# Kernel optimization log

Hardware: AMD Instinct MI355X
Metric: run time of the kernel (lower is better)

## Reference

```python
import jax, jax.numpy as jnp
import numpy as np

B, S, D, H = 4, 2048, 1024, 16
HD = D // H  # head_dim = 64


def setup_inputs() -> dict:
    key = jax.random.key(0)
    ks = jax.random.split(key, 10)
    scale = 1.0 / np.sqrt(D)
    x = jax.random.normal(ks[0], (B, S, D), dtype=jnp.float32)
    mask = jax.random.randint(ks[1], (B, S, S), 0, 2, dtype=jnp.int32)
    Wq = jax.random.normal(ks[2], (D, D), dtype=jnp.float32) * scale
    Wk = jax.random.normal(ks[3], (D, D), dtype=jnp.float32) * scale
    Wv = jax.random.normal(ks[4], (D, D), dtype=jnp.float32) * scale
    Wo = jax.random.normal(ks[5], (D, D), dtype=jnp.float32) * scale
    bq = jax.random.normal(ks[6], (D,), dtype=jnp.float32) * 0.01
    bk = jax.random.normal(ks[7], (D,), dtype=jnp.float32) * 0.01
    bv = jax.random.normal(ks[8], (D,), dtype=jnp.float32) * 0.01
    bo = jax.random.normal(ks[9], (D,), dtype=jnp.float32) * 0.01
    return {"x": x, "mask": mask, "Wq": Wq, "bq": bq, "Wk": Wk, "bk": bk,
            "Wv": Wv, "bv": bv, "Wo": Wo, "bo": bo}


def reference(x, mask, Wq, bq, Wk, bk, Wv, bv, Wo, bo):
    # QKV projections (nn.Linear: x @ W^T + b; W stored pre-transposed here as [D,D])
    q = x @ Wq + bq  # [B,S,D]
    k = x @ Wk + bk
    v = x @ Wv + bv
    # split heads -> [B,H,S,HD]
    def heads(t):
        return t.reshape(B, S, H, HD).transpose(0, 2, 1, 3)
    q, k, v = heads(q), heads(k), heads(v)
    scores = jnp.einsum('bhqd,bhkd->bhqk', q, k) / jnp.sqrt(jnp.float32(HD))
    # mask: [B,S,S] -> broadcast over heads; positions where mask==0 get -inf
    scores = jnp.where(mask[:, None, :, :] == 0, -jnp.inf, scores)
    attn = jax.nn.softmax(scores, axis=-1)
    attn = jnp.where(jnp.isnan(attn), 0.0, attn)  # nan_to_num(nan=0.0)
    out = jnp.einsum('bhqk,bhkd->bhqd', attn, v)  # [B,H,S,HD]
    out = out.transpose(0, 2, 1, 3).reshape(B, S, D)
    return out @ Wo + bo
```

## Files before the change

### kernel.cpp

```cpp
#include <hip/hip_runtime.h>
#include <hip/hip_bf16.h>
#include <stdint.h>

#define B_  4
#define S_  2048
#define D_  1024
#define H_  16
#define HD_ 64

typedef __attribute__((ext_vector_type(4))) float f32x4;
typedef __attribute__((ext_vector_type(8))) short bf16x8;

typedef const unsigned int __attribute__((address_space(1)))* gas_ptr;
typedef unsigned int __attribute__((address_space(3)))* las_ptr;

__device__ __forceinline__ void async16(const void* g, void* l) {
  __builtin_amdgcn_global_load_lds((gas_ptr)g, (las_ptr)l, 16, 0, 0);
}

__global__ __launch_bounds__(256) void cvt_x(const float* __restrict__ in,
                                             __hip_bfloat16* __restrict__ out,
                                             int n) {
  const int i = (blockIdx.x * blockDim.x + threadIdx.x) * 4;
  if (i >= n) return;
  const float4 v = *(const float4*)(in + i);
  union { ushort4 u; __hip_bfloat16 h[4]; } o;
  o.h[0] = (__hip_bfloat16)v.x;
  o.h[1] = (__hip_bfloat16)v.y;
  o.h[2] = (__hip_bfloat16)v.z;
  o.h[3] = (__hip_bfloat16)v.w;
  *(ushort4*)(out + i) = o.u;
}

__global__ __launch_bounds__(256) void pack_mask(const int* __restrict__ mk,
                                                 unsigned long long* __restrict__ bits) {
  const long long i = (long long)blockIdx.x * 256 + threadIdx.x;
  const unsigned long long b = __ballot(mk[i] != 0);
  if ((threadIdx.x & 63) == 0) bits[i >> 6] = b;
}

__global__ void transpose_w(const float* __restrict__ Wq,
                            const float* __restrict__ Wk,
                            const float* __restrict__ Wv,
                            const float* __restrict__ Wo,
                            __hip_bfloat16* __restrict__ Wt_qkv,
                            __hip_bfloat16* __restrict__ Wt_o) {
  __shared__ float t[32][33];
  const int z = blockIdx.z;
  const float* W = (z == 0) ? Wq : (z == 1) ? Wk : (z == 2) ? Wv : Wo;
  __hip_bfloat16* Wt = (z < 3) ? (Wt_qkv + (size_t)z * D_ * D_) : Wt_o;
  const int x = blockIdx.x * 32 + threadIdx.x;
  const int y = blockIdx.y * 32 + threadIdx.y;
  t[threadIdx.y][threadIdx.x] = W[(size_t)y * D_ + x];
  __syncthreads();
  const int xo = blockIdx.y * 32 + threadIdx.x;
  const int yo = blockIdx.x * 32 + threadIdx.y;
  Wt[(size_t)yo * D_ + xo] = (__hip_bfloat16)t[threadIdx.x][threadIdx.y];
}

__global__ __launch_bounds__(256) void gemm_qkv(
    const __hip_bfloat16* __restrict__ A,
    const __hip_bfloat16* __restrict__ Bt,
    const float* __restrict__ bq,
    const float* __restrict__ bk,
    const float* __restrict__ bv,
    __hip_bfloat16* __restrict__ QKo,
    __hip_bfloat16* __restrict__ Vt) {
  __shared__ __hip_bfloat16 sA[128 * 32];
  __shared__ __hip_bfloat16 sB[128 * 32];
  const int K = 1024;
  const int tid  = threadIdx.x;
  const int wave = tid >> 6;
  const int lane = tid & 63;
  const int quad = lane >> 4;
  const int l16  = lane & 15;
  const int bm = blockIdx.y * 128;
  const int bn = blockIdx.x * 128;
  const int wm = (wave >> 1) * 64;
  const int wn = (wave & 1) * 64;

  const int r0 = wave * 2, r1 = wave * 2 + 1;
  const int lrow = lane >> 2;
  const int lcol = (lane & 3) * 8;

  const __hip_bfloat16* ga0 = A  + (size_t)(bm + r0 * 16 + lrow) * K + lcol;
  const __hip_bfloat16* ga1 = A  + (size_t)(bm + r1 * 16 + lrow) * K + lcol;
  const __hip_bfloat16* gb0 = Bt + (size_t)(bn + r0 * 16 + lrow) * K + lcol;
  const __hip_bfloat16* gb1 = Bt + (size_t)(bn + r1 * 16 + lrow) * K + lcol;
  char* la0 = (char*)sA + r0 * 1024;
  char* la1 = (char*)sA + r1 * 1024;
  char* lb0 = (char*)sB + r0 * 1024;
  char* lb1 = (char*)sB + r1 * 1024;

  const char* pa = (const char*)sA + (wm + l16) * 64 + quad * 16;
  const char* pb = (const char*)sB + (wn + l16) * 64 + quad * 16;

  f32x4 acc[4][4] = {};

  for (int k0 = 0; k0 < K; k0 += 32) {
    async16(ga0 + k0, la0);
    async16(ga1 + k0, la1);
    async16(gb0 + k0, lb0);
    async16(gb1 + k0, lb1);
    __syncthreads();
    bf16x8 af[4], bf[4];
#pragma unroll
    for (int mt = 0; mt < 4; ++mt) af[mt] = *(const bf16x8*)(pa + mt * 1024);
#pragma unroll
    for (int nt = 0; nt < 4; ++nt) bf[nt] = *(const bf16x8*)(pb + nt * 1024);
#pragma unroll
    for (int mt = 0; mt < 4; ++mt)
#pragma unroll
      for (int nt = 0; nt < 4; ++nt)
        acc[mt][nt] = __builtin_amdgcn_mfma_f32_16x16x32_bf16(af[mt], bf[nt], acc[mt][nt], 0, 0, 0);
    __syncthreads();
  }

#pragma unroll
  for (int mt = 0; mt < 4; ++mt) {
    const int row = bm + wm + mt * 16 + quad * 4;
#pragma unroll
    for (int nt = 0; nt < 4; ++nt) {
      const int col = bn + wn + nt * 16 + l16;
      f32x4 v = acc[mt][nt];
      if (col < 2048) {
        const float bias = (col < 1024) ? bq[col] : bk[col - 1024];
        const float sc = (col < 1024) ? 0.18033688011f : 1.0f;
#pragma unroll
        for (int r = 0; r < 4; ++r)
          QKo[(size_t)(row + r) * 2048 + col] = (__hip_bfloat16)((v[r] + bias) * sc);
      } else {
        const int cv = col - 2048;
        const float bias = bv[cv];
        const int hh = cv >> 6, d = cv & 63;
        const int bb = row >> 11, s0 = row & 2047;
        union { __hip_bfloat16 h[4]; unsigned long long u; } pk;
#pragma unroll
        for (int r = 0; r < 4; ++r) pk.h[r] = (__hip_bfloat16)(v[r] + bias);
        *(unsigned long long*)(Vt + ((size_t)(bb * 16 + hh) * 64 + d) * 2048 + s0) = pk.u;
      }
    }
  }
}

__global__ __launch_bounds__(256) void gemm_out(
    const __hip_bfloat16* __restrict__ A,
    const __hip_bfloat16* __restrict__ Bt,
    const float* __restrict__ b0,
    float* __restrict__ C,
    int N, int K) {
  __shared__ __hip_bfloat16 sA[128 * 32];
  __shared__ __hip_bfloat16 sB[128 * 32];
  const int tid  = threadIdx.x;
  const int wave = tid >> 6;
  const int lane = tid & 63;
  const int quad = lane >> 4;
  const int l16  = lane & 15;
  const int bm = blockIdx.y * 128;
  const int bn = blockIdx.x * 128;
  const int wm = (wave >> 1) * 64;
  const int wn = (wave & 1) * 64;

  const int r0 = wave * 2, r1 = wave * 2 + 1;
  const int lrow = lane >> 2;
  const int lcol = (lane & 3) * 8;

  const __hip_bfloat16* ga0 = A  + (size_t)(bm + r0 * 16 + lrow) * K + lcol;
  const __hip_bfloat16* ga1 = A  + (size_t)(bm + r1 * 16 + lrow) * K + lcol;
  const __hip_bfloat16* gb0 = Bt + (size_t)(bn + r0 * 16 + lrow) * K + lcol;
  const __hip_bfloat16* gb1 = Bt + (size_t)(bn + r1 * 16 + lrow) * K + lcol;
  char* la0 = (char*)sA + r0 * 1024;
  char* la1 = (char*)sA + r1 * 1024;
  char* lb0 = (char*)sB + r0 * 1024;
  char* lb1 = (char*)sB + r1 * 1024;

  const char* pa = (const char*)sA + (wm + l16) * 64 + quad * 16;
  const char* pb = (const char*)sB + (wn + l16) * 64 + quad * 16;

  f32x4 acc[4][4] = {};

  for (int k0 = 0; k0 < K; k0 += 32) {
    async16(ga0 + k0, la0);
    async16(ga1 + k0, la1);
    async16(gb0 + k0, lb0);
    async16(gb1 + k0, lb1);
    __syncthreads();
    bf16x8 af[4], bf[4];
#pragma unroll
    for (int mt = 0; mt < 4; ++mt) af[mt] = *(const bf16x8*)(pa + mt * 1024);
#pragma unroll
    for (int nt = 0; nt < 4; ++nt) bf[nt] = *(const bf16x8*)(pb + nt * 1024);
#pragma unroll
    for (int mt = 0; mt < 4; ++mt)
#pragma unroll
      for (int nt = 0; nt < 4; ++nt)
        acc[mt][nt] = __builtin_amdgcn_mfma_f32_16x16x32_bf16(af[mt], bf[nt], acc[mt][nt], 0, 0, 0);
    __syncthreads();
  }

#pragma unroll
  for (int mt = 0; mt < 4; ++mt) {
    const int row = bm + wm + mt * 16 + quad * 4;
#pragma unroll
    for (int nt = 0; nt < 4; ++nt) {
      const int col = bn + wn + nt * 16 + l16;
      const float bias = b0[col];
      f32x4 v = acc[mt][nt];
#pragma unroll
      for (int r = 0; r < 4; ++r)
        C[(size_t)(row + r) * N + col] = v[r] + bias;
    }
  }
}

__global__ __launch_bounds__(256, 4) void flash_attn(
    const __hip_bfloat16* __restrict__ QK,
    const __hip_bfloat16* __restrict__ Vt,
    const unsigned long long* __restrict__ mbits,
    __hip_bfloat16* __restrict__ O) {
  __shared__ __hip_bfloat16 sK[2][64 * 64];
  __shared__ __hip_bfloat16 sV[2][64 * 64];
  __shared__ __hip_bfloat16 sP[4][16 * 64];

  const int qt = blockIdx.x, h = blockIdx.y, b = blockIdx.z;
  const int tid = threadIdx.x;
  const int wave = tid >> 6, lane = tid & 63, quad = lane >> 4, l16 = lane & 15;
  const int qbase = qt * 128;
  const size_t brow = (size_t)b * S_;
  const int bh = b * H_ + h;

  bf16x8 qf[2][2];
#pragma unroll
  for (int g = 0; g < 2; ++g) {
    const __hip_bfloat16* qrow =
        QK + (brow + qbase + g * 64 + wave * 16 + l16) * 2048 + h * 64;
#pragma unroll
    for (int c = 0; c < 2; ++c)
      qf[g][c] = *(const bf16x8*)(qrow + c * 32 + quad * 8);
  }

  const int srow = lane >> 3;
  const int schk = (lane & 7) ^ srow;
  const __hip_bfloat16* gk0 =
      QK + (brow + wave * 16 + srow) * 2048 + 1024 + h * 64 + schk * 8;
  const __hip_bfloat16* gk1 = gk0 + (size_t)8 * 2048;
  const __hip_bfloat16* gv0 =
      Vt + ((size_t)bh * 64 + wave * 16 + srow) * 2048 + schk * 8;
  const __hip_bfloat16* gv1 = gv0 + (size_t)8 * 2048;
  char* const lK[2] = {(char*)&sK[0][0] + wave * 2048, (char*)&sK[1][0] + wave * 2048};
  char* const lV[2] = {(char*)&sV[0][0] + wave * 2048, (char*)&sV[1][0] + wave * 2048};

  const unsigned long long* mb0 = mbits + (brow + qbase + wave * 16 + l16) * 32;
  const unsigned long long* mb1 = mb0 + (size_t)64 * 32;

  const int xl = l16 & 7;
  const int koff0 = ((quad ^ xl) * 16);
  const int rowb = l16 * 128;

  float lst[2] = {0.f, 0.f};
  f32x4 oacc[2][4] = {};

  async16(gk0, lK[0]);
  async16(gk1, lK[0] + 1024);
  async16(gv0, lV[0]);
  async16(gv1, lV[0] + 1024);
  unsigned long long pm0 = mb0[0], pm1 = mb1[0];
  gk0 += (size_t)64 * 2048; gk1 += (size_t)64 * 2048;
  gv0 += 64; gv1 += 64;
  __syncthreads();

  const int NT = S_ / 64;
  for (int kt = 0; kt < NT; ++kt) {
    const int cur = kt & 1, nxt = cur ^ 1;

    if (kt + 1 < NT) {
      async16(gk0, lK[nxt]);
      async16(gk1, lK[nxt] + 1024);
      async16(gv0, lV[nxt]);
      async16(gv1, lV[nxt] + 1024);
      gk0 += (size_t)64 * 2048; gk1 += (size_t)64 * 2048;
      gv0 += 64; gv1 += 64;
    }
    const unsigned long long mw0 = pm0;
    const unsigned long long mw1 = pm1;
    const int kn = (kt + 1 < NT) ? kt + 1 : kt;
    pm0 = mb0[kn];
    pm1 = mb1[kn];

    const char* bK = (const char*)&sK[cur][0] + rowb;
    f32x4 st[2][4];
#pragma unroll
    for (int mt = 0; mt < 4; ++mt) {
      const bf16x8 kf0 = *(const bf16x8*)(bK + mt * 2048 + koff0);
      const bf16x8 kf1 = *(const bf16x8*)(bK + mt * 2048 + (koff0 ^ 64));
      f32x4 a0 = {}, a1 = {};
      a0 = __builtin_amdgcn_mfma_f32_16x16x32_bf16(kf0, qf[0][0], a0, 0, 0, 0);
      a0 = __builtin_amdgcn_mfma_f32_16x16x32_bf16(kf1, qf[0][1], a0, 0, 0, 0);
      a1 = __builtin_amdgcn_mfma_f32_16x16x32_bf16(kf0, qf[1][0], a1, 0, 0, 0);
      a1 = __builtin_amdgcn_mfma_f32_16x16x32_bf16(kf1, qf[1][1], a1, 0, 0, 0);
      st[0][mt] = a0;
      st[1][mt] = a1;
    }

    char* const sPw = (char*)&sP[wave][0];
    bf16x8 pf[2][2];
#pragma unroll
    for (int g = 0; g < 2; ++g) {
      const unsigned long long mw = (g == 0) ? mw0 : mw1;
      const unsigned lo = (unsigned)mw >> (quad * 4);
      const unsigned hi = (unsigned)(mw >> 32) >> (quad * 4);
      float sum = 0.f;
      union { __hip_bfloat16 h[4]; unsigned long long u; } pk[4];
#pragma unroll
      for (int mt = 0; mt < 4; ++mt) {
        const unsigned w32 = (mt < 2) ? lo : hi;
#pragma unroll
        for (int r = 0; r < 4; ++r) {
          float p = __builtin_amdgcn_exp2f(st[g][mt][r]);
          const bool ok = (w32 >> ((mt & 1) * 16 + r)) & 1u;
          p = ok ? p : 0.f;
          sum += p;
          pk[mt].h[r] = (__hip_bfloat16)p;
        }
      }
      lst[g] += sum;
#pragma unroll
      for (int mt = 0; mt < 4; ++mt)
        *(unsigned long long*)(sPw + rowb +
                               (((mt * 2 + (quad >> 1)) ^ xl) * 16) +
                               (quad & 1) * 8) = pk[mt].u;
      pf[g][0] = *(const bf16x8*)(sPw + rowb + koff0);
      pf[g][1] = *(const bf16x8*)(sPw + rowb + (koff0 ^ 64));
    }

    const char* bV = (const char*)&sV[cur][0] + rowb;
#pragma unroll
    for (int ht = 0; ht < 4; ++ht) {
      const bf16x8 vf0 = *(const bf16x8*)(bV + ht * 2048 + koff0);
      const bf16x8 vf1 = *(const bf16x8*)(bV + ht * 2048 + (koff0 ^ 64));
      oacc[0][ht] = __builtin_amdgcn_mfma_f32_16x16x32_bf16(vf0, pf[0][0], oacc[0][ht], 0, 0, 0);
      oacc[0][ht] = __builtin_amdgcn_mfma_f32_16x16x32_bf16(vf1, pf[0][1], oacc[0][ht], 0, 0, 0);
      oacc[1][ht] = __builtin_amdgcn_mfma_f32_16x16x32_bf16(vf0, pf[1][0], oacc[1][ht], 0, 0, 0);
      oacc[1][ht] = __builtin_amdgcn_mfma_f32_16x16x32_bf16(vf1, pf[1][1], oacc[1][ht], 0, 0, 0);
    }

    __syncthreads();
  }

#pragma unroll
  for (int g = 0; g < 2; ++g) {
    float l = lst[g];
    l += __shfl_xor(l, 16);
    l += __shfl_xor(l, 32);
    const float inv = (l > 0.f) ? 1.f / l : 0.f;
    __hip_bfloat16* orow =
        O + (brow + qbase + g * 64 + wave * 16 + l16) * 1024 + h * 64;
#pragma unroll
    for (int ht = 0; ht < 4; ++ht) {
      union { __hip_bfloat16 h[4]; unsigned long long u; } ok_;
#pragma unroll
      for (int r = 0; r < 4; ++r) ok_.h[r] = (__hip_bfloat16)(oacc[g][ht][r] * inv);
      *(unsigned long long*)(orow + ht * 16 + quad * 4) = ok_.u;
    }
  }
}

extern "C" void kernel_launch(void* const* d_in, const int* in_sizes, int n_in,
                              void* d_out, int out_size, void* d_ws, size_t ws_size,
                              hipStream_t stream) {
  const float* x  = (const float*)d_in[0];
  const int*   mk = (const int*)d_in[1];
  const float* Wq = (const float*)d_in[2];
  const float* bq = (const float*)d_in[3];
  const float* Wk = (const float*)d_in[4];
  const float* bk = (const float*)d_in[5];
  const float* Wv = (const float*)d_in[6];
  const float* bv = (const float*)d_in[7];
  const float* Wo = (const float*)d_in[8];
  const float* bo = (const float*)d_in[9];
  float* out = (float*)d_out;

  __hip_bfloat16* X16    = (__hip_bfloat16*)d_ws;
  __hip_bfloat16* Wt_qkv = X16 + (size_t)B_ * S_ * D_;
  __hip_bfloat16* Wt_o   = Wt_qkv + (size_t)3 * D_ * D_;
  __hip_bfloat16* QK     = Wt_o + (size_t)D_ * D_;
  __hip_bfloat16* Vt     = QK + (size_t)B_ * S_ * 2 * D_;
  __hip_bfloat16* Obuf   = Vt + (size_t)B_ * H_ * HD_ * S_;
  unsigned long long* mbits = (unsigned long long*)(Obuf + (size_t)B_ * S_ * D_);

  const int nx = B_ * S_ * D_;
  cvt_x<<<dim3((nx / 4 + 255) / 256), 256, 0, stream>>>(x, X16, nx);
  transpose_w<<<dim3(32, 32, 4), dim3(32, 32), 0, stream>>>(Wq, Wk, Wv, Wo, Wt_qkv, Wt_o);
  pack_mask<<<dim3((int)((size_t)B_ * S_ * S_ / 256)), 256, 0, stream>>>(mk, mbits);
  gemm_qkv<<<dim3(3 * D_ / 128, B_ * S_ / 128), 256, 0, stream>>>(
      X16, Wt_qkv, bq, bk, bv, QK, Vt);
  flash_attn<<<dim3(S_ / 128, H_, B_), 256, 0, stream>>>(QK, Vt, mbits, Obuf);
  gemm_out<<<dim3(D_ / 128, B_ * S_ / 128), 256, 0, stream>>>(
      Obuf, Wt_o, bo, out, D_, D_);
}
```

Before: 394.7 us.

## Replace LDS round-trip for P with permlane swaps and interleave softmax with MFMA

Removes the per-wave shared-memory staging buffer used to transpose the probability tile into the B-operand layout for the PV MFMA. Register lane permutes (v_permlane32/16_swap) produce the same layout instead. The exp/mask work is also moved inside the QK^T loop so it can overlap with the MFMAs, and s_setprio raises wave priority around the MFMA sections. This cuts LDS writes, reads and their waits, but correctness depends on the permlane layout exactly matching the old swizzled layout.

```diff
diff --git a/kernel.cpp b/kernel.cpp
--- a/kernel.cpp
+++ b/kernel.cpp
@@ -220,7 +220,6 @@
     __hip_bfloat16* __restrict__ O) {
   __shared__ __hip_bfloat16 sK[2][64 * 64];
   __shared__ __hip_bfloat16 sV[2][64 * 64];
-  __shared__ __hip_bfloat16 sP[4][16 * 64];
 
   const int qt = blockIdx.x, h = blockIdx.y, b = blockIdx.z;
   const int tid = threadIdx.x;
@@ -288,52 +287,60 @@
     pm1 = mb1[kn];
 
     const char* bK = (const char*)&sK[cur][0] + rowb;
-    f32x4 st[2][4];
+    unsigned pl[2][4][2];
+    float ps[2][4];
 #pragma unroll
     for (int mt = 0; mt < 4; ++mt) {
       const bf16x8 kf0 = *(const bf16x8*)(bK + mt * 2048 + koff0);
       const bf16x8 kf1 = *(const bf16x8*)(bK + mt * 2048 + (koff0 ^ 64));
       f32x4 a0 = {}, a1 = {};
+      __builtin_amdgcn_s_setprio(1);
       a0 = __builtin_amdgcn_mfma_f32_16x16x32_bf16(kf0, qf[0][0], a0, 0, 0, 0);
       a0 = __builtin_amdgcn_mfma_f32_16x16x32_bf16(kf1, qf[0][1], a0, 0, 0, 0);
       a1 = __builtin_amdgcn_mfma_f32_16x16x32_bf16(kf0, qf[1][0], a1, 0, 0, 0);
       a1 = __builtin_amdgcn_mfma_f32_16x16x32_bf16(kf1, qf[1][1], a1, 0, 0, 0);
-      st[0][mt] = a0;
-      st[1][mt] = a1;
-    }
-
-    char* const sPw = (char*)&sP[wave][0];
+      __builtin_amdgcn_s_setprio(0);
+#pragma unroll
+      for (int g = 0; g < 2; ++g) {
+        const unsigned long long mw = g ? mw1 : mw0;
+        const unsigned w32 =
+            ((mt < 2) ? (unsigned)mw : (unsigned)(mw >> 32)) >> (quad * 4);
+        const f32x4 av = g ? a1 : a0;
+        float pr[4];
+#pragma unroll
+        for (int r = 0; r < 4; ++r) {
+          const float p = __builtin_amdgcn_exp2f(av[r]);
+          pr[r] = ((w32 >> ((mt & 1) * 16 + r)) & 1u) ? p : 0.f;
+        }
+        union { __hip_bfloat16 h[2]; unsigned u; } c0, c1;
+        c0.h[0] = (__hip_bfloat16)pr[0]; c0.h[1] = (__hip_bfloat16)pr[1];
+        c1.h[0] = (__hip_bfloat16)pr[2]; c1.h[1] = (__hip_bfloat16)pr[3];
+        pl[g][mt][0] = c0.u;
+        pl[g][mt][1] = c1.u;
+        ps[g][mt] = (pr[0] + pr[1]) + (pr[2] + pr[3]);
+      }
+    }
+    lst[0] += (ps[0][0] + ps[0][1]) + (ps[0][2] + ps[0][3]);
+    lst[1] += (ps[1][0] + ps[1][1]) + (ps[1][2] + ps[1][3]);
+
     bf16x8 pf[2][2];
 #pragma unroll
-    for (int g = 0; g < 2; ++g) {
-      const unsigned long long mw = (g == 0) ? mw0 : mw1;
-      const unsigned lo = (unsigned)mw >> (quad * 4);
-      const unsigned hi = (unsigned)(mw >> 32) >> (quad * 4);
-      float sum = 0.f;
-      union { __hip_bfloat16 h[4]; unsigned long long u; } pk[4];
-#pragma unroll
-      for (int mt = 0; mt < 4; ++mt) {
-        const unsigned w32 = (mt < 2) ? lo : hi;
-#pragma unroll
-        for (int r = 0; r < 4; ++r) {
-          float p = __builtin_amdgcn_exp2f(st[g][mt][r]);
-          const bool ok = (w32 >> ((mt & 1) * 16 + r)) & 1u;
-          p = ok ? p : 0.f;
-          sum += p;
-          pk[mt].h[r] = (__hip_bfloat16)p;
-        }
+    for (int g = 0; g < 2; ++g)
+#pragma unroll
+      for (int c = 0; c < 2; ++c) {
+        unsigned e0 = pl[g][2 * c][0], o0 = pl[g][2 * c + 1][0];
+        unsigned e1 = pl[g][2 * c][1], o1 = pl[g][2 * c + 1][1];
+        asm("v_permlane32_swap_b32 %0, %1" : "+v"(e0), "+v"(o0));
+        asm("v_permlane16_swap_b32 %0, %1" : "+v"(e0), "+v"(o0));
+        asm("v_permlane32_swap_b32 %0, %1" : "+v"(e1), "+v"(o1));
+        asm("v_permlane16_swap_b32 %0, %1" : "+v"(e1), "+v"(o1));
+        union { unsigned u[4]; bf16x8 v; } uu;
+        uu.u[0] = e0; uu.u[1] = e1; uu.u[2] = o0; uu.u[3] = o1;
+        pf[g][c] = uu.v;
       }
-      lst[g] += sum;
-#pragma unroll
-      for (int mt = 0; mt < 4; ++mt)
-        *(unsigned long long*)(sPw + rowb +
-                               (((mt * 2 + (quad >> 1)) ^ xl) * 16) +
-                               (quad & 1) * 8) = pk[mt].u;
-      pf[g][0] = *(const bf16x8*)(sPw + rowb + koff0);
-      pf[g][1] = *(const bf16x8*)(sPw + rowb + (koff0 ^ 64));
-    }
 
     const char* bV = (const char*)&sV[cur][0] + rowb;
+    __builtin_amdgcn_s_setprio(1);
 #pragma unroll
     for (int ht = 0; ht < 4; ++ht) {
       const bf16x8 vf0 = *(const bf16x8*)(bV + ht * 2048 + koff0);
@@ -343,6 +350,7 @@
       oacc[1][ht] = __builtin_amdgcn_mfma_f32_16x16x32_bf16(vf0, pf[1][0], oacc[1][ht], 0, 0, 0);
       oacc[1][ht] = __builtin_amdgcn_mfma_f32_16x16x32_bf16(vf1, pf[1][1], oacc[1][ht], 0, 0, 0);
     }
+    __builtin_amdgcn_s_setprio(0);
 
     __syncthreads();
   }
```

After: 390.4 us. Within noise of the previous version (-1.1%).
